# Kernel tuning notes

Hardware: AMD Instinct MI355X
Metric: run time of the kernel (lower is better)

Reference implementation:

```python
import jax, jax.numpy as jnp
import numpy as np

N = 40000
E = 640000
D_RNA = 1000
D_PROT = 300
H = 64      # hidden_channels
OUT = 32    # out_channels
HEADS = 4


def setup_inputs() -> dict:
    key = jax.random.key(0)
    ks = jax.random.split(key, 24)
    s = 0.05
    w = lambda k, shape: jax.random.normal(k, shape, jnp.float32) * s
    inp = {
        'x': jax.random.normal(ks[0], (N, D_RNA + D_PROT), jnp.float32),
        'edge_index': jax.random.randint(ks[1], (2, E), 0, N, jnp.int32),
        'input_dim_rna': D_RNA,
        # embeddings
        'W_rna': w(ks[2], (D_RNA, H)), 'b_rna': jnp.zeros((H,), jnp.float32),
        'W_prot': w(ks[3], (D_PROT, H)), 'b_prot': jnp.zeros((H,), jnp.float32),
        # GATConv1: in 2H=128 -> heads*H=256
        'W1s': w(ks[4], (2 * H, HEADS * H)), 'W1d': w(ks[5], (2 * H, HEADS * H)),
        'att1_s': w(ks[6], (HEADS, H)), 'att1_d': w(ks[7], (HEADS, H)),
        'bias1': jnp.zeros((HEADS * H,), jnp.float32),
        # lin1: 2H -> heads*H
        'Wl1': w(ks[8], (2 * H, HEADS * H)), 'bl1': jnp.zeros((HEADS * H,), jnp.float32),
        # GATConv2: in heads*H=256 -> heads*OUT=128
        'W2s': w(ks[9], (HEADS * H, HEADS * OUT)), 'W2d': w(ks[10], (HEADS * H, HEADS * OUT)),
        'att2_s': w(ks[11], (HEADS, OUT)), 'att2_d': w(ks[12], (HEADS, OUT)),
        'bias2': jnp.zeros((HEADS * OUT,), jnp.float32),
        # lin2: heads*H -> heads*OUT
        'Wl2': w(ks[13], (HEADS * H, HEADS * OUT)), 'bl2': jnp.zeros((HEADS * OUT,), jnp.float32),
    }
    return inp


def _gat(x_in, edge_index, Ws, Wd, att_s, att_d, bias, heads, ch):
    # PyG GATConv, bipartite weights, add_self_loops=False, concat=True, eval (no dropout)
    n = x_in.shape[0]
    src, dst = edge_index[0], edge_index[1]
    xs = (x_in @ Ws).reshape(n, heads, ch)   # source projection
    xd = (x_in @ Wd).reshape(n, heads, ch)   # destination projection
    a_s = jnp.einsum('nhc,hc->nh', xs, att_s)  # [N,H]
    a_d = jnp.einsum('nhc,hc->nh', xd, att_d)  # [N,H]
    e = jax.nn.leaky_relu(a_s[src] + a_d[dst], 0.2)          # [E,H]
    m = jax.lax.stop_gradient(jax.ops.segment_max(e, dst, num_segments=n))
    p = jnp.exp(e - m[dst])
    denom = jax.ops.segment_sum(p, dst, num_segments=n)       # [N,H]
    alpha = p / denom[dst]                                    # segment softmax over incoming edges
    msg = xs[src] * alpha[:, :, None]                         # [E,H,C]
    agg = jax.ops.segment_sum(msg, dst, num_segments=n)       # [N,H,C]
    return agg.reshape(n, heads * ch) + bias


def reference(x, edge_index, input_dim_rna, W_rna, b_rna, W_prot, b_prot,
              W1s, W1d, att1_s, att1_d, bias1, Wl1, bl1,
              W2s, W2d, att2_s, att2_d, bias2, Wl2, bl2):
    x_rna = x[:, :input_dim_rna] @ W_rna + b_rna
    x_prot = x[:, input_dim_rna:] @ W_prot + b_prot
    h = jnp.concatenate([x_rna, x_prot], axis=1)              # [N, 2H]
    h = _gat(h, edge_index, W1s, W1d, att1_s, att1_d, bias1, HEADS, H) + h @ Wl1 + bl1
    h = jax.nn.relu(h)
    out = _gat(h, edge_index, W2s, W2d, att2_s, att2_d, bias2, HEADS, OUT) + h @ Wl2 + bl2
    return out
```

## Files before the change

kernel.cpp:

```cpp
#include <hip/hip_runtime.h>
#include <hip/hip_bf16.h>
#include <stdint.h>


#define HEADS 4
#define CH1   64
#define CH2   32
#define HC1   256
#define HC2   128

static constexpr int D_RNA  = 1000;
static constexpr int D_PROT = 300;
static constexpr int D_IN   = 1300;
static constexpr int HDIM   = 128;

typedef __bf16 bf16x8 __attribute__((ext_vector_type(8)));
typedef float  f32x4  __attribute__((ext_vector_type(4)));
typedef unsigned short ushort;

__device__ __forceinline__ float lrelu(float x) { return x >= 0.f ? x : 0.2f * x; }
__device__ __forceinline__ float bf2f(unsigned int u16) {
  return __uint_as_float(u16 << 16);
}
__device__ __forceinline__ ushort f2bf(float f) {
  union { float f; unsigned int u; } x; x.f = f;
  unsigned int r = x.u + 0x7fffu + ((x.u >> 16) & 1u);
  return (ushort)(r >> 16);
}

__global__ void zero_i32(int* p, int n) {
  int i = blockIdx.x * 256 + threadIdx.x;
  if (i < n) p[i] = 0;
}

__global__ void hist_kernel(const int* __restrict__ dstv, int* __restrict__ deg, int E) {
  int i = blockIdx.x * 256 + threadIdx.x;
  if (i < E) atomicAdd(&deg[dstv[i]], 1);
}

__global__ void scan_kernel(const int* __restrict__ deg, int* __restrict__ off,
                            int* __restrict__ cur, int n) {
  __shared__ int s[1024];
  int tid = threadIdx.x;
  const int CHK = (n + 1023) / 1024;
  int base = tid * CHK;
  int sum = 0;
  for (int j = 0; j < CHK; ++j) {
    int i = base + j;
    if (i < n) sum += deg[i];
  }
  s[tid] = sum;
  __syncthreads();
  for (int o = 1; o < 1024; o <<= 1) {
    int t = (tid >= o) ? s[tid - o] : 0;
    __syncthreads();
    s[tid] += t;
    __syncthreads();
  }
  int run = s[tid] - sum;
  for (int j = 0; j < CHK; ++j) {
    int i = base + j;
    if (i < n) {
      off[i] = run; cur[i] = run;
      run += deg[i];
    }
  }
  if (tid == 1023) off[n] = s[1023];
}

__global__ void scatter_kernel(const int* __restrict__ srcv, const int* __restrict__ dstv,
                               int* __restrict__ cur, int* __restrict__ srcs, int E) {
  int i = blockIdx.x * 256 + threadIdx.x;
  if (i < E) {
    int d = dstv[i];
    int pos = atomicAdd(&cur[d], 1);
    srcs[pos] = srcv[i];
  }
}

__global__ void fold_att_kernel(const float* __restrict__ W1s, const float* __restrict__ W1d,
                                const float* __restrict__ at1s, const float* __restrict__ at1d,
                                const float* __restrict__ W2s, const float* __restrict__ W2d,
                                const float* __restrict__ at2s, const float* __restrict__ at2d,
                                ushort* __restrict__ BTA1, ushort* __restrict__ BTA2) {
  int tid = blockIdx.x * blockDim.x + threadIdx.x;
  int stride = gridDim.x * blockDim.x;
  for (int o = tid; o < HDIM * HEADS; o += stride) {
    int k = o >> 2, h = o & 3;
    float ss = 0.f, sd = 0.f;
    for (int c = 0; c < CH1; ++c) {
      ss += W1s[k * HC1 + h * CH1 + c] * at1s[h * CH1 + c];
      sd += W1d[k * HC1 + h * CH1 + c] * at1d[h * CH1 + c];
    }
    ushort sh = f2bf(ss), dh = f2bf(sd);
    BTA1[(0 + h) * HDIM + k] = sh;
    BTA1[(4 + h) * HDIM + k] = f2bf(ss - bf2f(sh));
    BTA1[(8 + h) * HDIM + k] = dh;
    BTA1[(12 + h) * HDIM + k] = f2bf(sd - bf2f(dh));
  }
  for (int o = tid; o < HC1 * HEADS; o += stride) {
    int k = o >> 2, h = o & 3;
    float ss = 0.f, sd = 0.f;
    for (int c = 0; c < CH2; ++c) {
      ss += W2s[k * HC2 + h * CH2 + c] * at2s[h * CH2 + c];
      sd += W2d[k * HC2 + h * CH2 + c] * at2d[h * CH2 + c];
    }
    ushort sh = f2bf(ss), dh = f2bf(sd);
    BTA2[(0 + h) * HC1 + k] = sh;
    BTA2[(4 + h) * HC1 + k] = f2bf(ss - bf2f(sh));
    BTA2[(8 + h) * HC1 + k] = dh;
    BTA2[(12 + h) * HC1 + k] = f2bf(sd - bf2f(dh));
  }
  for (int i = tid; i < 48 * HDIM; i += stride) BTA1[16 * HDIM + i] = 0;
  for (int i = tid; i < 48 * HC1; i += stride) BTA2[16 * HC1 + i] = 0;
}

__global__ void convert_weights(const float* __restrict__ W_rna, const float* __restrict__ W_prot,
                                const float* __restrict__ W1s, const float* __restrict__ Wl1,
                                const float* __restrict__ W2s, const float* __restrict__ Wl2,
                                const float* __restrict__ b1, const float* __restrict__ bl1,
                                const float* __restrict__ b2, const float* __restrict__ bl2,
                                ushort* BTr, ushort* BTp, ushort* BT1, ushort* BT2,
                                float* biasL1, float* biasL2) {
  int tid = blockIdx.x * blockDim.x + threadIdx.x;
  int stride = gridDim.x * blockDim.x;
  for (int i = tid; i < 64 * 1024; i += stride) {
    int n = i >> 10, k = i & 1023;
    BTr[i] = (k < D_RNA) ? f2bf(W_rna[k * 64 + n]) : 0;
  }
  for (int i = tid; i < 64 * 320; i += stride) {
    int n = i / 320, k = i - n * 320;
    BTp[i] = (k < D_PROT) ? f2bf(W_prot[k * 64 + n]) : 0;
  }
  for (int i = tid; i < 512 * 128; i += stride) {
    int n = i >> 7, k = i & 127;
    BT1[i] = f2bf(n < 256 ? W1s[k * 256 + n] : Wl1[k * 256 + n - 256]);
  }
  for (int i = tid; i < 256 * 256; i += stride) {
    int n = i >> 8, k = i & 255;
    BT2[i] = f2bf(n < 128 ? W2s[k * 128 + n] : Wl2[k * 128 + n - 128]);
  }
  for (int i = tid; i < 512; i += stride) biasL1[i] = (i < 256) ? b1[i] : bl1[i - 256];
  for (int i = tid; i < 256; i += stride) biasL2[i] = (i < 128) ? b2[i] : bl2[i - 128];
}

#define LDK 72

__device__ __forceinline__ f32x4 mfma_bf16(bf16x8 a, bf16x8 b, f32x4 c) {
  return __builtin_amdgcn_mfma_f32_16x16x32_bf16(a, b, c, 0, 0, 0);
}

__launch_bounds__(256)
__global__ void embed_gemm(const float* __restrict__ x,
                           const ushort* __restrict__ BTr, const ushort* __restrict__ BTp,
                           const float* __restrict__ b_rna, const float* __restrict__ b_prot,
                           ushort* __restrict__ h0) {
  const bool prot = (blockIdx.x == 1);
  const int Kpad = prot ? 320 : 1024;
  const int acol = prot ? D_RNA : 0;
  const ushort* BT = prot ? BTp : BTr;
  const float* bias = prot ? b_prot : b_rna;
  const int r0 = blockIdx.y * 64;

  __shared__ ushort As[64 * LDK];
  __shared__ ushort Bs[64 * LDK];
  int tid = threadIdx.x;
  int wave = tid >> 6, lane = tid & 63;
  int quad = lane >> 4, lr = lane & 15;
  f32x4 acc[4];
#pragma unroll
  for (int c = 0; c < 4; ++c) acc[c] = (f32x4){0.f, 0.f, 0.f, 0.f};

  int srow = tid >> 2, skq = (tid & 3) * 16;
  const float* aprow = x + (size_t)(r0 + srow) * D_IN;
  const ushort* bprow = BT + (size_t)srow * Kpad;

  float4 fa[4];
  uint4 fb0, fb1;

  auto loadA = [&](int k0) {
#pragma unroll
    for (int q = 0; q < 4; ++q) {
      int kg = acol + k0 + skq + q * 4;
      fa[q] = (kg + 4 <= D_IN) ? *(const float4*)(aprow + kg)
                               : make_float4(0.f, 0.f, 0.f, 0.f);
    }
  };
  auto loadB = [&](int k0) {
    const ushort* bp = bprow + k0 + skq;
    fb0 = *(const uint4*)bp;
    fb1 = *(const uint4*)(bp + 8);
  };

  loadA(0);
  loadB(0);

  for (int k0 = 0; k0 < Kpad; k0 += 64) {
    {
      ushort tmp[16];
#pragma unroll
      for (int q = 0; q < 4; ++q) {
        tmp[q * 4 + 0] = f2bf(fa[q].x); tmp[q * 4 + 1] = f2bf(fa[q].y);
        tmp[q * 4 + 2] = f2bf(fa[q].z); tmp[q * 4 + 3] = f2bf(fa[q].w);
      }
      *(uint4*)&As[srow * LDK + skq] = *(const uint4*)&tmp[0];
      *(uint4*)&As[srow * LDK + skq + 8] = *(const uint4*)&tmp[8];
      *(uint4*)&Bs[srow * LDK + skq] = fb0;
      *(uint4*)&Bs[srow * LDK + skq + 8] = fb1;
    }
    __syncthreads();
    if (k0 + 64 < Kpad) {
      loadA(k0 + 64);
      loadB(k0 + 64);
    }
    int arow = wave * 16 + lr;
    bf16x8 a0 = *(const bf16x8*)&As[arow * LDK + quad * 8];
    bf16x8 a1 = *(const bf16x8*)&As[arow * LDK + 32 + quad * 8];
#pragma unroll
    for (int c = 0; c < 4; ++c) {
      bf16x8 b0 = *(const bf16x8*)&Bs[(c * 16 + lr) * LDK + quad * 8];
      bf16x8 b1 = *(const bf16x8*)&Bs[(c * 16 + lr) * LDK + 32 + quad * 8];
      acc[c] = mfma_bf16(a0, b0, acc[c]);
      acc[c] = mfma_bf16(a1, b1, acc[c]);
    }
    __syncthreads();
  }
  int colb = prot ? 64 : 0;
#pragma unroll
  for (int c = 0; c < 4; ++c) {
#pragma unroll
    for (int j = 0; j < 4; ++j) {
      int row = r0 + wave * 16 + quad * 4 + j;
      int col = c * 16 + lr;
      h0[(size_t)row * HDIM + colb + col] = f2bf(acc[c][j] + bias[col]);
    }
  }
}

__launch_bounds__(256)
__global__ void layer_gemm(const ushort* __restrict__ A, int K,
                           const ushort* __restrict__ BT, const float* __restrict__ bias,
                           ushort* __restrict__ out0, ushort* __restrict__ out1, int halfw,
                           const ushort* __restrict__ BTA,
                           float* __restrict__ a_s, float* __restrict__ a_d) {
  const bool att = (blockIdx.x == gridDim.x - 1);
  const int cb = att ? 0 : blockIdx.x * 128;
  const int r0 = blockIdx.y * 64;
  __shared__ ushort As[64 * LDK];
  __shared__ ushort Bs[2][64 * LDK];
  int tid = threadIdx.x;
  int wave = tid >> 6, lane = tid & 63;
  int quad = lane >> 4, lr = lane & 15;
  f32x4 acc[8];
#pragma unroll
  for (int c = 0; c < 8; ++c) acc[c] = (f32x4){0.f, 0.f, 0.f, 0.f};

  int srow = tid >> 2, skq = (tid & 3) * 16;
  const ushort* aprow = A + (size_t)(r0 + srow) * K;
  const ushort* bprow0 = att ? (BTA + (size_t)srow * K)
                             : (BT + (size_t)(cb + srow) * K);
  const ushort* bprow1 = BT + (size_t)(cb + 64 + srow) * K;

  uint4 fa0, fa1, fb00, fb01, fb10, fb11;
  auto loadAB = [&](int k0) {
    const ushort* ap = aprow + k0 + skq;
    fa0 = *(const uint4*)ap;
    fa1 = *(const uint4*)(ap + 8);
    const ushort* bp0 = bprow0 + k0 + skq;
    fb00 = *(const uint4*)bp0;
    fb01 = *(const uint4*)(bp0 + 8);
    if (!att) {
      const ushort* bp1 = bprow1 + k0 + skq;
      fb10 = *(const uint4*)bp1;
      fb11 = *(const uint4*)(bp1 + 8);
    }
  };

  loadAB(0);

  for (int k0 = 0; k0 < K; k0 += 64) {
    *(uint4*)&As[srow * LDK + skq] = fa0;
    *(uint4*)&As[srow * LDK + skq + 8] = fa1;
    *(uint4*)&Bs[0][srow * LDK + skq] = fb00;
    *(uint4*)&Bs[0][srow * LDK + skq + 8] = fb01;
    if (!att) {
      *(uint4*)&Bs[1][srow * LDK + skq] = fb10;
      *(uint4*)&Bs[1][srow * LDK + skq + 8] = fb11;
    }
    __syncthreads();
    if (k0 + 64 < K) loadAB(k0 + 64);
    int arow = wave * 16 + lr;
    bf16x8 a0 = *(const bf16x8*)&As[arow * LDK + quad * 8];
    bf16x8 a1 = *(const bf16x8*)&As[arow * LDK + 32 + quad * 8];
#pragma unroll
    for (int c = 0; c < 4; ++c) {
      bf16x8 b0 = *(const bf16x8*)&Bs[0][(c * 16 + lr) * LDK + quad * 8];
      bf16x8 b1 = *(const bf16x8*)&Bs[0][(c * 16 + lr) * LDK + 32 + quad * 8];
      acc[c] = mfma_bf16(a0, b0, acc[c]);
      acc[c] = mfma_bf16(a1, b1, acc[c]);
    }
    if (!att) {
#pragma unroll
      for (int c = 0; c < 4; ++c) {
        bf16x8 b0 = *(const bf16x8*)&Bs[1][(c * 16 + lr) * LDK + quad * 8];
        bf16x8 b1 = *(const bf16x8*)&Bs[1][(c * 16 + lr) * LDK + 32 + quad * 8];
        acc[4 + c] = mfma_bf16(a0, b0, acc[4 + c]);
        acc[4 + c] = mfma_bf16(a1, b1, acc[4 + c]);
      }
    }
    __syncthreads();
  }
  if (att) {
#pragma unroll
    for (int j = 0; j < 4; ++j) {
      int row = r0 + wave * 16 + quad * 4 + j;
      float v0 = acc[0][j];
      float sum = v0 + __shfl_xor(v0, 4);
      if (lr < 4)                    a_s[(size_t)row * 4 + lr] = sum;
      else if (lr >= 8 && lr < 12)   a_d[(size_t)row * 4 + (lr - 8)] = sum;
    }
    return;
  }
#pragma unroll
  for (int t = 0; t < 2; ++t) {
#pragma unroll
    for (int c = 0; c < 4; ++c) {
#pragma unroll
      for (int j = 0; j < 4; ++j) {
        int row = r0 + wave * 16 + quad * 4 + j;
        int cg = cb + t * 64 + c * 16 + lr;
        ushort v = f2bf(acc[t * 4 + c][j] + bias[cg]);
        if (cg < halfw) out0[(size_t)row * halfw + cg] = v;
        else            out1[(size_t)row * halfw + cg - halfw] = v;
      }
    }
  }
}

template <int VEC>
__device__ __forceinline__ void load_bf(const ushort* p, float* out);
template <>
__device__ __forceinline__ void load_bf<4>(const ushort* p, float* out) {
  uint2 q = *(const uint2*)p;
  out[0] = bf2f(q.x & 0xffffu); out[1] = bf2f(q.x >> 16);
  out[2] = bf2f(q.y & 0xffffu); out[3] = bf2f(q.y >> 16);
}
template <>
__device__ __forceinline__ void load_bf<2>(const ushort* p, float* out) {
  unsigned int q = *(const unsigned int*)p;
  out[0] = bf2f(q & 0xffffu); out[1] = bf2f(q >> 16);
}

template <int CH, int VEC, bool RELU, bool OUT_BF16>
__launch_bounds__(256)
__global__ void gat_fused_kernel(const int* __restrict__ off, const int* __restrict__ srcs,
                                 const float* __restrict__ a_s, const float* __restrict__ a_d,
                                 const ushort* __restrict__ xs,
                                 const float* __restrict__ bias,
                                 const ushort* __restrict__ skip,
                                 void* __restrict__ outv, int N) {
  const int HC = 4 * CH;
  int wave = threadIdx.x >> 6, lane = threadIdx.x & 63;
  int n = blockIdx.x * 4 + wave;
  if (n >= N) return;
  int h = lane >> 4;
  int c = (lane & 15) * VEC;
  int s0 = off[n], end = off[n + 1];
  float adn = a_d[(size_t)n * 4 + h];

  float m = -1e30f;
  int i = s0;
  for (; i + 4 <= end; i += 4) {
    float e0 = a_s[(size_t)srcs[i] * 4 + h];
    float e1 = a_s[(size_t)srcs[i + 1] * 4 + h];
    float e2 = a_s[(size_t)srcs[i + 2] * 4 + h];
    float e3 = a_s[(size_t)srcs[i + 3] * 4 + h];
    m = fmaxf(m, fmaxf(fmaxf(lrelu(e0 + adn), lrelu(e1 + adn)),
                       fmaxf(lrelu(e2 + adn), lrelu(e3 + adn))));
  }
  for (; i < end; ++i) m = fmaxf(m, lrelu(a_s[(size_t)srcs[i] * 4 + h] + adn));

  float s = 0.f;
  float acc[VEC];
#pragma unroll
  for (int v = 0; v < VEC; ++v) acc[v] = 0.f;
  for (i = s0; i + 2 <= end; i += 2) {
    int sA = srcs[i], sB = srcs[i + 1];
    float pA = __expf(lrelu(a_s[(size_t)sA * 4 + h] + adn) - m);
    float pB = __expf(lrelu(a_s[(size_t)sB * 4 + h] + adn) - m);
    s += pA + pB;
    float xA[VEC], xB[VEC];
    load_bf<VEC>(xs + (size_t)sA * HC + h * CH + c, xA);
    load_bf<VEC>(xs + (size_t)sB * HC + h * CH + c, xB);
#pragma unroll
    for (int v = 0; v < VEC; ++v) acc[v] += pA * xA[v] + pB * xB[v];
  }
  if (i < end) {
    int sA = srcs[i];
    float pA = __expf(lrelu(a_s[(size_t)sA * 4 + h] + adn) - m);
    s += pA;
    float xA[VEC];
    load_bf<VEC>(xs + (size_t)sA * HC + h * CH + c, xA);
#pragma unroll
    for (int v = 0; v < VEC; ++v) acc[v] += pA * xA[v];
  }

  float r = s > 0.f ? 1.f / s : 0.f;
  size_t obase = (size_t)n * HC + h * CH + c;
  float sk[VEC];
  load_bf<VEC>(skip + obase, sk);
#pragma unroll
  for (int v = 0; v < VEC; ++v) {
    float val = acc[v] * r + bias[h * CH + c + v] + sk[v];
    if (RELU) val = fmaxf(val, 0.f);
    if (OUT_BF16) ((ushort*)outv)[obase + v] = f2bf(val);
    else          ((float*)outv)[obase + v] = val;
  }
}

extern "C" void kernel_launch(void* const* d_in, const int* in_sizes, int n_in,
                              void* d_out, int out_size, void* d_ws, size_t ws_size,
                              hipStream_t stream) {
  const float* x      = (const float*)d_in[0];
  const int*   ei     = (const int*)d_in[1];
  const float* W_rna  = (const float*)d_in[3];
  const float* b_rna  = (const float*)d_in[4];
  const float* W_prot = (const float*)d_in[5];
  const float* b_prot = (const float*)d_in[6];
  const float* W1s    = (const float*)d_in[7];
  const float* W1d    = (const float*)d_in[8];
  const float* at1s   = (const float*)d_in[9];
  const float* at1d   = (const float*)d_in[10];
  const float* bias1  = (const float*)d_in[11];
  const float* Wl1    = (const float*)d_in[12];
  const float* bl1    = (const float*)d_in[13];
  const float* W2s    = (const float*)d_in[14];
  const float* W2d    = (const float*)d_in[15];
  const float* at2s   = (const float*)d_in[16];
  const float* at2d   = (const float*)d_in[17];
  const float* bias2  = (const float*)d_in[18];
  const float* Wl2    = (const float*)d_in[19];
  const float* bl2    = (const float*)d_in[20];

  const int N = in_sizes[0] / D_IN;
  const int E = in_sizes[1] / 2;
  const int* srcv = ei;
  const int* dstv = ei + E;

  char* ws = (char*)d_ws;
  size_t o = 0;
  auto carve = [&](size_t bytes) {
    void* p = ws + o;
    o += (bytes + 255) & ~(size_t)255;
    return p;
  };
  int* deg    = (int*)carve((size_t)N * 4);
  int* offp   = (int*)carve((size_t)(N + 1) * 4);
  int* cur    = (int*)carve((size_t)N * 4);
  int* srcs   = (int*)carve((size_t)E * 4);
  float* a_s  = (float*)carve((size_t)N * 4 * 4);
  float* a_d  = (float*)carve((size_t)N * 4 * 4);
  ushort* BTr = (ushort*)carve(64 * 1024 * 2);
  ushort* BTp = (ushort*)carve(64 * 320 * 2);
  ushort* BT1 = (ushort*)carve(512 * 128 * 2);
  ushort* BT2 = (ushort*)carve(256 * 256 * 2);
  ushort* BTA1 = (ushort*)carve(64 * 128 * 2);
  ushort* BTA2 = (ushort*)carve(64 * 256 * 2);
  float* biasL1 = (float*)carve(512 * 4);
  float* biasL2 = (float*)carve(256 * 4);
  ushort* h0  = (ushort*)carve((size_t)N * HDIM * 2);
  ushort* xs1 = (ushort*)carve((size_t)N * HC1 * 2);
  ushort* z1  = (ushort*)carve((size_t)N * HC1 * 2);
  ushort* h1  = (ushort*)carve((size_t)N * HC1 * 2);
  ushort* xs2 = h0;
  ushort* z2  = z1;
  float* out = (float*)d_out;

  zero_i32<<<(N + 255) / 256, 256, 0, stream>>>(deg, N);
  hist_kernel<<<(E + 255) / 256, 256, 0, stream>>>(dstv, deg, E);
  scan_kernel<<<1, 1024, 0, stream>>>(deg, offp, cur, N);
  scatter_kernel<<<(E + 255) / 256, 256, 0, stream>>>(srcv, dstv, cur, srcs, E);
  fold_att_kernel<<<8, 256, 0, stream>>>(W1s, W1d, at1s, at1d, W2s, W2d, at2s, at2d,
                                         BTA1, BTA2);
  convert_weights<<<256, 256, 0, stream>>>(W_rna, W_prot, W1s, Wl1, W2s, Wl2,
                                           bias1, bl1, bias2, bl2,
                                           BTr, BTp, BT1, BT2, biasL1, biasL2);
  embed_gemm<<<dim3(2, N / 64), 256, 0, stream>>>(x, BTr, BTp, b_rna, b_prot, h0);
  layer_gemm<<<dim3(5, N / 64), 256, 0, stream>>>(h0, HDIM, BT1, biasL1, xs1, z1, HC1,
                                                  BTA1, a_s, a_d);
  gat_fused_kernel<CH1, 4, true, true><<<N / 4, 256, 0, stream>>>(offp, srcs, a_s, a_d, xs1,
                                                                  bias1, z1, h1, N);
  layer_gemm<<<dim3(3, N / 64), 256, 0, stream>>>(h1, HC1, BT2, biasL2, xs2, z2, HC2,
                                                  BTA2, a_s, a_d);
  gat_fused_kernel<CH2, 2, false, false><<<N / 4, 256, 0, stream>>>(offp, srcs, a_s, a_d, xs2,
                                                                    bias2, z2, out, N);
}
```

Baseline: 700.7 us.

## Use online softmax and 8-wide bf16 loads in fused GAT aggregation

Replaces the two-pass segment softmax (a max pass, then an exp/accumulate pass) with a single-pass online softmax that rescales the running sum and accumulators whenever the max grows. This removes the second sweep over neighbor indices and attention scores. Each lane now handles 8 channels with 16-byte loads, so one wave covers 2 nodes in layer 1 and 4 nodes in layer 2, and the launch grids shrink to match. The costs are extra exp/rescale work when the max changes, and divergence within a wave when grouped nodes have different degrees.

Result: faster. 655.5 us (-6.5%).

```diff
diff --git a/kernel.cpp b/kernel.cpp
--- a/kernel.cpp
+++ b/kernel.cpp
@@ -337,21 +337,15 @@
   }
 }
 
-template <int VEC>
-__device__ __forceinline__ void load_bf(const ushort* p, float* out);
-template <>
-__device__ __forceinline__ void load_bf<4>(const ushort* p, float* out) {
-  uint2 q = *(const uint2*)p;
-  out[0] = bf2f(q.x & 0xffffu); out[1] = bf2f(q.x >> 16);
-  out[2] = bf2f(q.y & 0xffffu); out[3] = bf2f(q.y >> 16);
-}
-template <>
-__device__ __forceinline__ void load_bf<2>(const ushort* p, float* out) {
-  unsigned int q = *(const unsigned int*)p;
-  out[0] = bf2f(q & 0xffffu); out[1] = bf2f(q >> 16);
-}
-
-template <int CH, int VEC, bool RELU, bool OUT_BF16>
+__device__ __forceinline__ void load_bf8(const ushort* p, float* o) {
+  uint4 q = *(const uint4*)p;
+  o[0] = bf2f(q.x & 0xffffu); o[1] = bf2f(q.x >> 16);
+  o[2] = bf2f(q.y & 0xffffu); o[3] = bf2f(q.y >> 16);
+  o[4] = bf2f(q.z & 0xffffu); o[5] = bf2f(q.z >> 16);
+  o[6] = bf2f(q.w & 0xffffu); o[7] = bf2f(q.w >> 16);
+}
+
+template <int CH, bool RELU, bool OUT_BF16>
 __launch_bounds__(256)
 __global__ void gat_fused_kernel(const int* __restrict__ off, const int* __restrict__ srcs,
                                  const float* __restrict__ a_s, const float* __restrict__ a_d,
@@ -359,62 +353,82 @@
                                  const float* __restrict__ bias,
                                  const ushort* __restrict__ skip,
                                  void* __restrict__ outv, int N) {
-  const int HC = 4 * CH;
+  const int HC  = 4 * CH;
+  const int LPH = CH / 8;
+  const int LPN = 4 * LPH;
+  const int NPW = 64 / LPN;
   int wave = threadIdx.x >> 6, lane = threadIdx.x & 63;
-  int n = blockIdx.x * 4 + wave;
+  int g  = lane / LPN;
+  int hl = (lane % LPN) / LPH;
+  int li = lane % LPH;
+  int n = blockIdx.x * (4 * NPW) + wave * NPW + g;
   if (n >= N) return;
-  int h = lane >> 4;
-  int c = (lane & 15) * VEC;
-  int s0 = off[n], end = off[n + 1];
-  float adn = a_d[(size_t)n * 4 + h];
-
-  float m = -1e30f;
-  int i = s0;
-  for (; i + 4 <= end; i += 4) {
-    float e0 = a_s[(size_t)srcs[i] * 4 + h];
-    float e1 = a_s[(size_t)srcs[i + 1] * 4 + h];
-    float e2 = a_s[(size_t)srcs[i + 2] * 4 + h];
-    float e3 = a_s[(size_t)srcs[i + 3] * 4 + h];
-    m = fmaxf(m, fmaxf(fmaxf(lrelu(e0 + adn), lrelu(e1 + adn)),
-                       fmaxf(lrelu(e2 + adn), lrelu(e3 + adn))));
-  }
-  for (; i < end; ++i) m = fmaxf(m, lrelu(a_s[(size_t)srcs[i] * 4 + h] + adn));
-
-  float s = 0.f;
-  float acc[VEC];
-#pragma unroll
-  for (int v = 0; v < VEC; ++v) acc[v] = 0.f;
-  for (i = s0; i + 2 <= end; i += 2) {
+  int i = off[n], end = off[n + 1];
+  float adn = a_d[(size_t)n * 4 + hl];
+  const int cofs = hl * CH + li * 8;
+
+  float m = -1e30f, s = 0.f;
+  float acc[8];
+#pragma unroll
+  for (int v = 0; v < 8; ++v) acc[v] = 0.f;
+
+  for (; i + 2 <= end; i += 2) {
     int sA = srcs[i], sB = srcs[i + 1];
-    float pA = __expf(lrelu(a_s[(size_t)sA * 4 + h] + adn) - m);
-    float pB = __expf(lrelu(a_s[(size_t)sB * 4 + h] + adn) - m);
+    float eA = lrelu(a_s[(size_t)sA * 4 + hl] + adn);
+    float eB = lrelu(a_s[(size_t)sB * 4 + hl] + adn);
+    float xA[8], xB[8];
+    load_bf8(xs + (size_t)sA * HC + cofs, xA);
+    load_bf8(xs + (size_t)sB * HC + cofs, xB);
+    float mn = fmaxf(m, fmaxf(eA, eB));
+    if (mn > m) {
+      float f = __expf(m - mn);
+      s *= f;
+#pragma unroll
+      for (int v = 0; v < 8; ++v) acc[v] *= f;
+      m = mn;
+    }
+    float pA = __expf(eA - m), pB = __expf(eB - m);
     s += pA + pB;
-    float xA[VEC], xB[VEC];
-    load_bf<VEC>(xs + (size_t)sA * HC + h * CH + c, xA);
-    load_bf<VEC>(xs + (size_t)sB * HC + h * CH + c, xB);
-#pragma unroll
-    for (int v = 0; v < VEC; ++v) acc[v] += pA * xA[v] + pB * xB[v];
+#pragma unroll
+    for (int v = 0; v < 8; ++v) acc[v] += pA * xA[v] + pB * xB[v];
   }
   if (i < end) {
     int sA = srcs[i];
-    float pA = __expf(lrelu(a_s[(size_t)sA * 4 + h] + adn) - m);
+    float eA = lrelu(a_s[(size_t)sA * 4 + hl] + adn);
+    float xA[8];
+    load_bf8(xs + (size_t)sA * HC + cofs, xA);
+    if (eA > m) {
+      float f = __expf(m - eA);
+      s *= f;
+#pragma unroll
+      for (int v = 0; v < 8; ++v) acc[v] *= f;
+      m = eA;
+    }
+    float pA = __expf(eA - m);
     s += pA;
-    float xA[VEC];
-    load_bf<VEC>(xs + (size_t)sA * HC + h * CH + c, xA);
-#pragma unroll
-    for (int v = 0; v < VEC; ++v) acc[v] += pA * xA[v];
+#pragma unroll
+    for (int v = 0; v < 8; ++v) acc[v] += pA * xA[v];
   }
 
   float r = s > 0.f ? 1.f / s : 0.f;
-  size_t obase = (size_t)n * HC + h * CH + c;
-  float sk[VEC];
-  load_bf<VEC>(skip + obase, sk);
-#pragma unroll
-  for (int v = 0; v < VEC; ++v) {
-    float val = acc[v] * r + bias[h * CH + c + v] + sk[v];
-    if (RELU) val = fmaxf(val, 0.f);
-    if (OUT_BF16) ((ushort*)outv)[obase + v] = f2bf(val);
-    else          ((float*)outv)[obase + v] = val;
+  size_t obase = (size_t)n * HC + cofs;
+  float sk[8];
+  load_bf8(skip + obase, sk);
+  float val[8];
+#pragma unroll
+  for (int v = 0; v < 8; ++v) {
+    val[v] = acc[v] * r + bias[cofs + v] + sk[v];
+    if (RELU) val[v] = fmaxf(val[v], 0.f);
+  }
+  if (OUT_BF16) {
+    ushort o8[8];
+#pragma unroll
+    for (int v = 0; v < 8; ++v) o8[v] = f2bf(val[v]);
+    *(uint4*)&((ushort*)outv)[obase] = *(const uint4*)o8;
+  } else {
+    float* op = (float*)outv + obase;
+    *(float4*)op = make_float4(val[0], val[1], val[2], val[3]);
+    *(float4*)(op + 4) = make_float4(val[4], val[5], val[6], val[7]);
   }
 }
 
@@ -488,10 +502,10 @@
   embed_gemm<<<dim3(2, N / 64), 256, 0, stream>>>(x, BTr, BTp, b_rna, b_prot, h0);
   layer_gemm<<<dim3(5, N / 64), 256, 0, stream>>>(h0, HDIM, BT1, biasL1, xs1, z1, HC1,
                                                   BTA1, a_s, a_d);
-  gat_fused_kernel<CH1, 4, true, true><<<N / 4, 256, 0, stream>>>(offp, srcs, a_s, a_d, xs1,
-                                                                  bias1, z1, h1, N);
+  gat_fused_kernel<CH1, true, true><<<N / 8, 256, 0, stream>>>(offp, srcs, a_s, a_d, xs1,
+                                                               bias1, z1, h1, N);
   layer_gemm<<<dim3(3, N / 64), 256, 0, stream>>>(h1, HC1, BT2, biasL2, xs2, z2, HC2,
                                                   BTA2, a_s, a_d);
-  gat_fused_kernel<CH2, 2, false, false><<<N / 4, 256, 0, stream>>>(offp, srcs, a_s, a_d, xs2,
-                                                                    bias2, z2, out, N);
-}
+  gat_fused_kernel<CH2, false, false><<<N / 16, 256, 0, stream>>>(offp, srcs, a_s, a_d, xs2,
+                                                                  bias2, z2, out, N);
+}
```
